# Kernel tuning notes

Hardware: AMD Instinct MI355X
Metric: run time of the kernel (lower is better)

## Reference

```python
import jax, jax.numpy as jnp
import numpy as np

N_NODES = 50000
N_EDGES = 800000
N_FEAT = 128
N_HID = 128
N_LAYER = 4
N_CLASS = 40


def setup_inputs() -> dict:
    key = jax.random.key(0)
    ks = jax.random.split(key, 8)
    x = jax.random.normal(ks[0], (N_NODES, N_FEAT), jnp.float32)
    edge_index = jax.random.randint(ks[1], (2, N_EDGES), 0, N_NODES, dtype=jnp.int64)
    s = 1.0 / np.float32(np.sqrt(N_HID))
    # n_feat == n_hid so all L conv weights stack into one [L, C, C] tensor
    convW = jax.random.normal(ks[2], (N_LAYER, N_HID, N_HID), jnp.float32) * s
    convb = jnp.zeros((N_LAYER, N_HID), jnp.float32)
    W_att = jax.random.normal(ks[3], (N_HID, N_HID), jnp.float32) * s
    a_att = jax.random.normal(ks[4], (N_HID,), jnp.float32) * s
    W_out = jax.random.normal(ks[5], (N_HID, N_CLASS), jnp.float32) * s
    b_out = jnp.zeros((N_CLASS,), jnp.float32)
    return dict(x=x, edge_index=edge_index, convW=convW, convb=convb,
                W_att=W_att, a_att=a_att, W_out=W_out, b_out=b_out)


def reference(x, edge_index, convW, convb, W_att, a_att, W_out, b_out):
    src, dst = edge_index[0], edge_index[1]
    N = x.shape[0]
    # GCN symmetric normalization with self-loops: deg = 1 + in-degree
    deg = jax.ops.segment_sum(jnp.ones_like(dst, dtype=jnp.float32), dst,
                              num_segments=N) + 1.0
    dinv = jax.lax.rsqrt(deg)
    enorm = (dinv[src] * dinv[dst])[:, None]   # per-edge norm
    snorm = (dinv * dinv)[:, None]             # self-loop norm

    hs = []
    h = x
    for l in range(N_LAYER):
        hW = h @ convW[l]                                          # [N, C]
        agg = jax.ops.segment_sum(hW[src] * enorm, dst, num_segments=N)
        agg = agg + hW * snorm                                     # self-loop
        h = jax.nn.relu(agg + convb[l])
        # dropout is identity at inference (training=False)
        hs.append(h)

    H = jnp.stack(hs, axis=1)                                      # [N, L, C]
    # additive attention over layers: alpha_l = softmax_l(a . tanh(W h_l))
    scores = jnp.tanh(H @ W_att) @ a_att                           # [N, L]
    alpha = jax.nn.softmax(scores, axis=1)
    fused = jnp.einsum('nl,nlc->nc', alpha, H)                     # [N, C]
    return fused @ W_out + b_out                                   # [N, n_class]
```

## Files before the change

kernel.cpp:

```cpp
#include <hip/hip_runtime.h>

#define NNODES 50000
#define NEDGES 800000
#define NCLASS 40
#define CNTB  3125
#define PREPB 320
#define WOUTB 24
#define GEMMB 782
#define XBLK  3125
#define WELL  64

typedef _Float16 half8  __attribute__((ext_vector_type(8)));
typedef float    floatx4 __attribute__((ext_vector_type(4)));

#define CSTR 136
#define SMEM_BYTES (64 * CSTR * 2 + 256)

__device__ __forceinline__ float fast_tanh(float x) {
    return 1.0f - 2.0f / (__expf(2.0f * x) + 1.0f);
}

__global__ __launch_bounds__(256) void k_pre(const int* __restrict__ src, const int* __restrict__ dst,
                                             int* __restrict__ cnt, int* __restrict__ esrc,
                                             const float* __restrict__ convW, const float* __restrict__ W_att,
                                             _Float16* __restrict__ WT,
                                             const float* __restrict__ Wout, _Float16* __restrict__ WoutT) {
    int bid = blockIdx.x, tid = threadIdx.x;
    if (bid < CNTB) {
        int e = bid * 256 + tid;
        int d = dst[e];
        int slot = atomicAdd(&cnt[d], 1);
        esrc[d * WELL + slot] = src[e];
    } else if (bid < CNTB + PREPB) {
        int idx = (bid - CNTB) * 256 + tid;
        int mat = idx >> 14, rem = idx & 16383;
        int j = rem & 7, lane = (rem >> 3) & 63, tile = rem >> 9;
        int l15 = lane & 15, quad = lane >> 4;
        int ct = tile & 7, kk = tile >> 3;
        int n = ct * 16 + l15, k = kk * 32 + quad * 8 + j;
        const float* s = (mat < 4) ? (convW + mat * 16384) : W_att;
        WT[idx] = (_Float16)s[k * 128 + n];
    } else {
        int idx = (bid - CNTB - PREPB) * 256 + tid;
        int j = idx & 7, lane = (idx >> 3) & 63, tile = idx >> 9;
        int l15 = lane & 15, quad = lane >> 4;
        int ct = tile % 3, kk = tile / 3;
        int n = ct * 16 + l15, k = kk * 32 + quad * 8 + j;
        WoutT[idx] = (n < NCLASS) ? (_Float16)Wout[k * NCLASS + n] : (_Float16)0.f;
    }
}

__global__ __launch_bounds__(256) void k_gemm0(const float* __restrict__ Av, const _Float16* __restrict__ WTf,
                                               const int* __restrict__ cnt, _Float16* __restrict__ C) {
    __shared__ __align__(16) char smem[SMEM_BYTES];
    _Float16 (*Csh)[CSTR] = (_Float16 (*)[CSTR])smem;
    float* sdinv = (float*)(smem + 64 * CSTR * 2);
    int m0 = blockIdx.x * 64;
    int tid = threadIdx.x;
    int wave = tid >> 6, lane = tid & 63;
    int quad = lane >> 4, l15 = lane & 15;
    int ko = quad * 8;

    if (tid < 64) {
        int r = m0 + tid; if (r > NNODES - 1) r = NNODES - 1;
        sdinv[tid] = rsqrtf((float)cnt[r] + 1.0f);
    }

    floatx4 acc[4][2];
#pragma unroll
    for (int rt = 0; rt < 4; ++rt)
#pragma unroll
        for (int ct = 0; ct < 2; ++ct) acc[rt][ct] = (floatx4){0.f, 0.f, 0.f, 0.f};

#pragma unroll
    for (int kk = 0; kk < 4; ++kk) {
        half8 a[4], b[2];
#pragma unroll
        for (int rt = 0; rt < 4; ++rt) {
            int row = m0 + rt * 16 + l15;
            if (row > NNODES - 1) row = NNODES - 1;
            const float* Ap = Av + (size_t)row * 128 + kk * 32 + ko;
            float4 f0 = *(const float4*)Ap;
            float4 f1 = *(const float4*)(Ap + 4);
            a[rt] = (half8){(_Float16)f0.x, (_Float16)f0.y, (_Float16)f0.z, (_Float16)f0.w,
                            (_Float16)f1.x, (_Float16)f1.y, (_Float16)f1.z, (_Float16)f1.w};
        }
#pragma unroll
        for (int ct = 0; ct < 2; ++ct)
            b[ct] = *(const half8*)&WTf[((kk * 8 + (wave * 2 + ct)) * 64 + lane) * 8];
#pragma unroll
        for (int rt = 0; rt < 4; ++rt)
#pragma unroll
            for (int ct = 0; ct < 2; ++ct)
                acc[rt][ct] = __builtin_amdgcn_mfma_f32_16x16x32_f16(a[rt], b[ct], acc[rt][ct], 0, 0, 0);
    }
    __syncthreads();

#pragma unroll
    for (int rt = 0; rt < 4; ++rt)
#pragma unroll
        for (int r = 0; r < 4; ++r) {
            float d = sdinv[rt * 16 + quad * 4 + r];
#pragma unroll
            for (int ct = 0; ct < 2; ++ct)
                Csh[rt * 16 + quad * 4 + r][wave * 32 + ct * 16 + l15] = (_Float16)(acc[rt][ct][r] * d);
        }
    __syncthreads();

    int row = tid >> 2, seg = tid & 3;
    int gm = m0 + row;
    if (gm < NNODES) {
#pragma unroll
        for (int j = 0; j < 4; ++j)
            *(half8*)(C + (size_t)gm * 128 + seg * 32 + j * 8) = *(const half8*)&Csh[row][seg * 32 + j * 8];
    }
}

template <bool HAS_GEMM>
__global__ __launch_bounds__(128) void k_layer(const _Float16* __restrict__ hin,
                                               const int* __restrict__ cnt, const int* __restrict__ esrc,
                                               const float* __restrict__ bias,
                                               _Float16* __restrict__ hh,
                                               const _Float16* __restrict__ WTatt, const float* __restrict__ a_att,
                                               float* __restrict__ scores, int layer,
                                               const _Float16* __restrict__ WTnext, _Float16* __restrict__ hout) {
    __shared__ __align__(16) _Float16 h[16][CSTR];
    __shared__ float bsh[128];
    __shared__ float sdv[16];
    __shared__ float pp[2][16];
    int tid = threadIdx.x;
    bsh[tid] = bias[tid];
    int wave = tid >> 6, lane = tid & 63;
    int n0 = blockIdx.x * 16;

    {
        int nl = tid >> 3;
        int cl = tid & 7;
        int c16 = cl * 16;
        int n = n0 + nl;
        int cv = cnt[n];
        int beg = n * WELL, end = beg + cv;
        float dn = rsqrtf((float)cv + 1.0f);
        const _Float16* sp = hin + (size_t)n * 128 + c16;
        half8 sv0 = *(const half8*)sp;
        half8 sv1 = *(const half8*)(sp + 8);

        float a[16];
#pragma unroll
        for (int u = 0; u < 16; ++u) a[u] = 0.f;

        int idxA[4]; float mskA[4];
#pragma unroll
        for (int i = 0; i < 4; ++i) {
            int ei = beg + i;
            int t = esrc[ei];
            bool ok = ei < end;
            idxA[i] = ok ? t : n;
            mskA[i] = ok ? 1.f : 0.f;
        }
        for (int e = beg; e < end; e += 4) {
            half8 v0[4], v1[4];
#pragma unroll
            for (int i = 0; i < 4; ++i) {
                const _Float16* p = hin + (size_t)idxA[i] * 128 + c16;
                v0[i] = *(const half8*)p;
                v1[i] = *(const half8*)(p + 8);
            }
            int idxB[4]; float mskB[4];
#pragma unroll
            for (int i = 0; i < 4; ++i) {
                int ei = e + 4 + i;
                int t = esrc[ei];
                bool ok = ei < end;
                idxB[i] = ok ? t : n;
                mskB[i] = ok ? 1.f : 0.f;
            }
#pragma unroll
            for (int i = 0; i < 4; ++i) {
                float m = mskA[i];
#pragma unroll
                for (int u = 0; u < 8; ++u) {
                    a[u]     += m * (float)v0[i][u];
                    a[8 + u] += m * (float)v1[i][u];
                }
            }
#pragma unroll
            for (int i = 0; i < 4; ++i) { idxA[i] = idxB[i]; mskA[i] = mskB[i]; }
        }
        __syncthreads();
        half8 o0, o1;
#pragma unroll
        for (int u = 0; u < 8; ++u) {
            float r0 = (a[u]     + (float)sv0[u]) * dn + bsh[c16 + u];
            float r1 = (a[8 + u] + (float)sv1[u]) * dn + bsh[c16 + 8 + u];
            o0[u] = (_Float16)fmaxf(r0, 0.f);
            o1[u] = (_Float16)fmaxf(r1, 0.f);
        }
        *(half8*)(hh + (size_t)n * 128 + c16)     = o0;
        *(half8*)(hh + (size_t)n * 128 + c16 + 8) = o1;
        *(half8*)&h[nl][c16]     = o0;
        *(half8*)&h[nl][c16 + 8] = o1;
        if (cl == 0) sdv[nl] = dn;
    }
    __syncthreads();

    int quad = lane >> 4, l15 = lane & 15;
    int ko = quad * 8;
    half8 af[4];
#pragma unroll
    for (int kk = 0; kk < 4; ++kk) af[kk] = *(const half8*)&h[l15][kk * 32 + ko];

    {
        float p[4] = {0.f, 0.f, 0.f, 0.f};
#pragma unroll
        for (int c2 = 0; c2 < 4; ++c2) {
            int ct = wave * 4 + c2;
            half8 b[4];
#pragma unroll
            for (int kk = 0; kk < 4; ++kk)
                b[kk] = *(const half8*)&WTatt[((kk * 8 + ct) * 64 + lane) * 8];
            floatx4 acc = (floatx4){0.f, 0.f, 0.f, 0.f};
#pragma unroll
            for (int kk = 0; kk < 4; ++kk)
                acc = __builtin_amdgcn_mfma_f32_16x16x32_f16(af[kk], b[kk], acc, 0, 0, 0);
            float av = a_att[ct * 16 + l15];
#pragma unroll
            for (int r = 0; r < 4; ++r) p[r] += av * fast_tanh(acc[r]);
        }
#pragma unroll
        for (int r = 0; r < 4; ++r) {
            float v = p[r];
            v += __shfl_xor(v, 1); v += __shfl_xor(v, 2);
            v += __shfl_xor(v, 4); v += __shfl_xor(v, 8);
            if (l15 == 0) pp[wave][quad * 4 + r] = v;
        }
    }
    __syncthreads();
    if (tid < 16) scores[(size_t)(n0 + tid) * 4 + layer] = pp[0][tid] + pp[1][tid];

    if (HAS_GEMM) {
        floatx4 acc[4];
#pragma unroll
        for (int c2 = 0; c2 < 4; ++c2) acc[c2] = (floatx4){0.f, 0.f, 0.f, 0.f};
#pragma unroll
        for (int c2 = 0; c2 < 4; ++c2) {
            int ct = wave * 4 + c2;
#pragma unroll
            for (int kk = 0; kk < 4; ++kk) {
                half8 b = *(const half8*)&WTnext[((kk * 8 + ct) * 64 + lane) * 8];
                acc[c2] = __builtin_amdgcn_mfma_f32_16x16x32_f16(af[kk], b, acc[c2], 0, 0, 0);
            }
        }
        __syncthreads();
#pragma unroll
        for (int c2 = 0; c2 < 4; ++c2) {
            int col = wave * 64 + c2 * 16 + l15;
#pragma unroll
            for (int r = 0; r < 4; ++r) {
                int row = quad * 4 + r;
                h[row][col] = (_Float16)(acc[c2][r] * sdv[row]);
            }
        }
        __syncthreads();
        int row = tid >> 3, seg = tid & 7;
        int gm = n0 + row;
        *(half8*)(hout + (size_t)gm * 128 + seg * 16)     = *(const half8*)&h[row][seg * 16];
        *(half8*)(hout + (size_t)gm * 128 + seg * 16 + 8) = *(const half8*)&h[row][seg * 16 + 8];
    }
}

__global__ __launch_bounds__(256) void k_fuse_out(const _Float16* __restrict__ hbase, const float* __restrict__ scores,
                                                  const _Float16* __restrict__ WoutT, const float* __restrict__ bout,
                                                  float* __restrict__ out) {
    __shared__ __align__(16) _Float16 Fs[64][136];
    __shared__ float salpha[256];
    const size_t LSTR = (size_t)NNODES * 128;
    int tid = threadIdx.x;
    int n0 = blockIdx.x * 64;

    if (tid < 64) {
        int node = n0 + tid; if (node > NNODES - 1) node = NNODES - 1;
        float4 s = *(const float4*)(scores + (size_t)node * 4);
        float mx = fmaxf(fmaxf(s.x, s.y), fmaxf(s.z, s.w));
        float e0 = __expf(s.x - mx), e1 = __expf(s.y - mx), e2 = __expf(s.z - mx), e3 = __expf(s.w - mx);
        float inv = 1.0f / (e0 + e1 + e2 + e3);
        salpha[tid * 4 + 0] = e0 * inv; salpha[tid * 4 + 1] = e1 * inv;
        salpha[tid * 4 + 2] = e2 * inv; salpha[tid * 4 + 3] = e3 * inv;
    }
    __syncthreads();

    {
        int no = tid >> 2, seg = tid & 3;
        int node = n0 + no; if (node > NNODES - 1) node = NNODES - 1;
        float al0 = salpha[no * 4 + 0], al1 = salpha[no * 4 + 1];
        float al2 = salpha[no * 4 + 2], al3 = salpha[no * 4 + 3];
        const _Float16* hp = hbase + (size_t)node * 128 + seg * 32;
#pragma unroll
        for (int j = 0; j < 4; ++j) {
            half8 h0 = *(const half8*)(hp + 0 * LSTR + j * 8);
            half8 h1 = *(const half8*)(hp + 1 * LSTR + j * 8);
            half8 h2 = *(const half8*)(hp + 2 * LSTR + j * 8);
            half8 h3 = *(const half8*)(hp + 3 * LSTR + j * 8);
            half8 f;
#pragma unroll
            for (int u = 0; u < 8; ++u)
                f[u] = (_Float16)(al0 * (float)h0[u] + al1 * (float)h1[u] +
                                  al2 * (float)h2[u] + al3 * (float)h3[u]);
            *(half8*)&Fs[no][seg * 32 + j * 8] = f;
        }
    }
    __syncthreads();

    int wave = tid >> 6, lane = tid & 63;
    int quad = lane >> 4, l15 = lane & 15;
    int ko = quad * 8;
    half8 ff[4];
    int frow = wave * 16 + l15;
#pragma unroll
    for (int kk = 0; kk < 4; ++kk) ff[kk] = *(const half8*)&Fs[frow][kk * 32 + ko];
#pragma unroll
    for (int ct = 0; ct < 3; ++ct) {
        half8 bw[4];
#pragma unroll
        for (int kk = 0; kk < 4; ++kk)
            bw[kk] = *(const half8*)(WoutT + ((kk * 3 + ct) * 64 + lane) * 8);
        floatx4 acc = (floatx4){0.f, 0.f, 0.f, 0.f};
#pragma unroll
        for (int kk = 0; kk < 4; ++kk)
            acc = __builtin_amdgcn_mfma_f32_16x16x32_f16(ff[kk], bw[kk], acc, 0, 0, 0);
        int col = ct * 16 + l15;
        if (col < NCLASS) {
            float bv = bout[col];
#pragma unroll
            for (int r = 0; r < 4; ++r) {
                int node = n0 + wave * 16 + quad * 4 + r;
                if (node < NNODES) out[(size_t)node * NCLASS + col] = acc[r] + bv;
            }
        }
    }
}

extern "C" void kernel_launch(void* const* d_in, const int* in_sizes, int n_in,
                              void* d_out, int out_size, void* d_ws, size_t ws_size,
                              hipStream_t stream) {
    const float* x     = (const float*)d_in[0];
    const int*   ei    = (const int*)d_in[1];
    const float* convW = (const float*)d_in[2];
    const float* convb = (const float*)d_in[3];
    const float* W_att = (const float*)d_in[4];
    const float* a_att = (const float*)d_in[5];
    const float* W_out = (const float*)d_in[6];
    const float* b_out = (const float*)d_in[7];
    float* out = (float*)d_out;

    char* ws = (char*)d_ws;
    size_t off = 0;
    auto take = [&](size_t nbytes) { char* p = ws + off; off += (nbytes + 255) & ~(size_t)255; return p; };
    int*       cnt     = (int*)take(NNODES * 4);
    int*       esrc    = (int*)take((size_t)NNODES * WELL * 4 + 1024);
    _Float16*  WoutT   = (_Float16*)take((size_t)48 * 128 * 2);
    float*     scores  = (float*)take(NNODES * 4 * 4);
    _Float16*  WT      = (_Float16*)take((size_t)5 * 128 * 128 * 2);
    _Float16*  hWsA    = (_Float16*)take((size_t)NNODES * 128 * 2);
    _Float16*  hh[4];
    for (int l = 0; l < 4; ++l) hh[l] = (_Float16*)take((size_t)NNODES * 128 * 2);
    _Float16*  hWsB    = (_Float16*)take((size_t)NNODES * 128 * 2);

    const int* src = ei;
    const int* dst = ei + NEDGES;

    hipMemsetAsync(cnt, 0, NNODES * 4, stream);
    k_pre<<<CNTB + PREPB + WOUTB, 256, 0, stream>>>(src, dst, cnt, esrc, convW, W_att, WT, W_out, WoutT);
    k_gemm0<<<GEMMB, 256, 0, stream>>>(x, WT, cnt, hWsA);

    k_layer<true><<<XBLK, 128, 0, stream>>>(hWsA, cnt, esrc, convb + 0 * 128, hh[0],
                                            WT + 4 * 16384, a_att, scores, 0, WT + 1 * 16384, hWsB);
    k_layer<true><<<XBLK, 128, 0, stream>>>(hWsB, cnt, esrc, convb + 1 * 128, hh[1],
                                            WT + 4 * 16384, a_att, scores, 1, WT + 2 * 16384, hWsA);
    k_layer<true><<<XBLK, 128, 0, stream>>>(hWsA, cnt, esrc, convb + 2 * 128, hh[2],
                                            WT + 4 * 16384, a_att, scores, 2, WT + 3 * 16384, hWsB);
    k_layer<false><<<XBLK, 128, 0, stream>>>(hWsB, cnt, esrc, convb + 3 * 128, hh[3],
                                             WT + 4 * 16384, a_att, scores, 3, (const _Float16*)nullptr,
                                             (_Float16*)nullptr);
    k_fuse_out<<<GEMMB, 256, 0, stream>>>(hh[0], scores, WoutT, b_out, out);
}
```

Measured before the change: 326.7 us.

## Replace global-atomic edge bucketing with two-level bucketed partition and local build

```diff
diff --git a/kernel.cpp b/kernel.cpp
--- a/kernel.cpp
+++ b/kernel.cpp
@@ -3,13 +3,18 @@
 #define NNODES 50000
 #define NEDGES 800000
 #define NCLASS 40
-#define CNTB  3125
-#define PREPB 320
-#define WOUTB 24
 #define GEMMB 782
 #define XBLK  3125
 #define WELL  64
 
+#define EBLK  782
+#define PREPB 80
+#define WOUTB 6
+#define BSHIFT 10
+#define NB    49
+#define NCNT  (NB * EBLK)
+#define SCANB 38
+
 typedef _Float16 half8  __attribute__((ext_vector_type(8)));
 typedef float    floatx4 __attribute__((ext_vector_type(4)));
 
@@ -20,19 +25,21 @@
     return 1.0f - 2.0f / (__expf(2.0f * x) + 1.0f);
 }
 
-__global__ __launch_bounds__(256) void k_pre(const int* __restrict__ src, const int* __restrict__ dst,
-                                             int* __restrict__ cnt, int* __restrict__ esrc,
-                                             const float* __restrict__ convW, const float* __restrict__ W_att,
-                                             _Float16* __restrict__ WT,
-                                             const float* __restrict__ Wout, _Float16* __restrict__ WoutT) {
+__global__ __launch_bounds__(1024) void k_hist(const int* __restrict__ dst, int* __restrict__ counts,
+                                               const float* __restrict__ convW, const float* __restrict__ W_att,
+                                               _Float16* __restrict__ WT,
+                                               const float* __restrict__ Wout, _Float16* __restrict__ WoutT) {
     int bid = blockIdx.x, tid = threadIdx.x;
-    if (bid < CNTB) {
-        int e = bid * 256 + tid;
-        int d = dst[e];
-        int slot = atomicAdd(&cnt[d], 1);
-        esrc[d * WELL + slot] = src[e];
-    } else if (bid < CNTB + PREPB) {
-        int idx = (bid - CNTB) * 256 + tid;
+    if (bid < EBLK) {
+        __shared__ int hist[NB];
+        if (tid < NB) hist[tid] = 0;
+        __syncthreads();
+        int e = bid * 1024 + tid;
+        if (e < NEDGES) atomicAdd(&hist[dst[e] >> BSHIFT], 1);
+        __syncthreads();
+        if (tid < NB) counts[tid * EBLK + bid] = hist[tid];
+    } else if (bid < EBLK + PREPB) {
+        int idx = (bid - EBLK) * 1024 + tid;
         int mat = idx >> 14, rem = idx & 16383;
         int j = rem & 7, lane = (rem >> 3) & 63, tile = rem >> 9;
         int l15 = lane & 15, quad = lane >> 4;
@@ -41,13 +48,91 @@
         const float* s = (mat < 4) ? (convW + mat * 16384) : W_att;
         WT[idx] = (_Float16)s[k * 128 + n];
     } else {
-        int idx = (bid - CNTB - PREPB) * 256 + tid;
+        int idx = (bid - EBLK - PREPB) * 1024 + tid;
         int j = idx & 7, lane = (idx >> 3) & 63, tile = idx >> 9;
         int l15 = lane & 15, quad = lane >> 4;
         int ct = tile % 3, kk = tile / 3;
         int n = ct * 16 + l15, k = kk * 32 + quad * 8 + j;
         WoutT[idx] = (n < NCLASS) ? (_Float16)Wout[k * NCLASS + n] : (_Float16)0.f;
     }
+}
+
+__global__ __launch_bounds__(1024) void k_bsum(const int* __restrict__ counts, int* __restrict__ bsum) {
+    int t = threadIdx.x, b = blockIdx.x;
+    int i = b * 1024 + t;
+    int v = (i < NCNT) ? counts[i] : 0;
+    v += __shfl_xor(v, 1);  v += __shfl_xor(v, 2);  v += __shfl_xor(v, 4);
+    v += __shfl_xor(v, 8);  v += __shfl_xor(v, 16); v += __shfl_xor(v, 32);
+    __shared__ int ws[16];
+    if ((t & 63) == 0) ws[t >> 6] = v;
+    __syncthreads();
+    if (t == 0) {
+        int s = 0;
+#pragma unroll
+        for (int w = 0; w < 16; ++w) s += ws[w];
+        bsum[b] = s;
+    }
+}
+
+__global__ __launch_bounds__(1024) void k_scan(int* __restrict__ counts, const int* __restrict__ bsum) {
+    __shared__ int part[1024];
+    __shared__ int ws[16];
+    int t = threadIdx.x, b = blockIdx.x;
+    int i = b * 1024 + t;
+    int c = (i < NCNT) ? counts[i] : 0;
+    int pv = (t < b) ? bsum[t] : 0;
+    pv += __shfl_xor(pv, 1);  pv += __shfl_xor(pv, 2);  pv += __shfl_xor(pv, 4);
+    pv += __shfl_xor(pv, 8);  pv += __shfl_xor(pv, 16); pv += __shfl_xor(pv, 32);
+    if ((t & 63) == 0) ws[t >> 6] = pv;
+    part[t] = c;
+    __syncthreads();
+    int boff = 0;
+#pragma unroll
+    for (int w = 0; w < 16; ++w) boff += ws[w];
+#pragma unroll
+    for (int d = 1; d < 1024; d <<= 1) {
+        int v = (t >= d) ? part[t - d] : 0;
+        __syncthreads();
+        part[t] += v;
+        __syncthreads();
+    }
+    if (i < NCNT) counts[i] = boff + part[t] - c;
+}
+
+__global__ __launch_bounds__(1024) void k_part(const int* __restrict__ src, const int* __restrict__ dst,
+                                               const int* __restrict__ counts, int2* __restrict__ ebuf) {
+    __shared__ int hist2[NB];
+    int bid = blockIdx.x, tid = threadIdx.x;
+    if (tid < NB) hist2[tid] = 0;
+    __syncthreads();
+    int e = bid * 1024 + tid;
+    if (e < NEDGES) {
+        int d = dst[e];
+        int s = src[e];
+        int b = d >> BSHIFT;
+        int slot = atomicAdd(&hist2[b], 1);
+        int pos = counts[b * EBLK + bid] + slot;
+        ebuf[pos] = make_int2(s, d);
+    }
+}
+
+__global__ __launch_bounds__(1024) void k_build(const int* __restrict__ counts, const int2* __restrict__ ebuf,
+                                                int* __restrict__ esrc, int* __restrict__ cnt) {
+    __shared__ int lcnt[1024];
+    int b = blockIdx.x, t = threadIdx.x;
+    lcnt[t] = 0;
+    __syncthreads();
+    int n0 = b << BSHIFT;
+    int lo = counts[b * EBLK];
+    int hi = (b < NB - 1) ? counts[(b + 1) * EBLK] : NEDGES;
+    for (int i = lo + t; i < hi; i += 1024) {
+        int2 p = ebuf[i];
+        int slot = atomicAdd(&lcnt[p.y - n0], 1);
+        esrc[p.y * WELL + slot] = p.x;
+    }
+    __syncthreads();
+    int n = n0 + t;
+    if (n < NNODES) cnt[n] = lcnt[t];
 }
 
 __global__ __launch_bounds__(256) void k_gemm0(const float* __restrict__ Av, const _Float16* __restrict__ WTf,
@@ -357,6 +442,9 @@
     size_t off = 0;
     auto take = [&](size_t nbytes) { char* p = ws + off; off += (nbytes + 255) & ~(size_t)255; return p; };
     int*       cnt     = (int*)take(NNODES * 4);
+    int*       counts  = (int*)take((size_t)NCNT * 4);
+    int*       bsum    = (int*)take(SCANB * 4);
+    int2*      ebuf    = (int2*)take((size_t)NEDGES * 8);
     int*       esrc    = (int*)take((size_t)NNODES * WELL * 4 + 1024);
     _Float16*  WoutT   = (_Float16*)take((size_t)48 * 128 * 2);
     float*     scores  = (float*)take(NNODES * 4 * 4);
@@ -369,8 +457,11 @@
     const int* src = ei;
     const int* dst = ei + NEDGES;
 
-    hipMemsetAsync(cnt, 0, NNODES * 4, stream);
-    k_pre<<<CNTB + PREPB + WOUTB, 256, 0, stream>>>(src, dst, cnt, esrc, convW, W_att, WT, W_out, WoutT);
+    k_hist<<<EBLK + PREPB + WOUTB, 1024, 0, stream>>>(dst, counts, convW, W_att, WT, W_out, WoutT);
+    k_bsum<<<SCANB, 1024, 0, stream>>>(counts, bsum);
+    k_scan<<<SCANB, 1024, 0, stream>>>(counts, bsum);
+    k_part<<<EBLK, 1024, 0, stream>>>(src, dst, counts, ebuf);
+    k_build<<<NB, 1024, 0, stream>>>(counts, ebuf, esrc, cnt);
     k_gemm0<<<GEMMB, 256, 0, stream>>>(x, WT, cnt, hWsA);
 
     k_layer<true><<<XBLK, 128, 0, stream>>>(hWsA, cnt, esrc, convb + 0 * 128, hh[0],
```

New measurement: 303.4 us. 7.1% less time.

## Build destination-bucketed edge lists via two-pass partition instead of global atomics

Applied to the files above, without the earlier changes.

```diff
diff --git a/kernel.cpp b/kernel.cpp
--- a/kernel.cpp
+++ b/kernel.cpp
@@ -3,13 +3,17 @@
 #define NNODES 50000
 #define NEDGES 800000
 #define NCLASS 40
-#define CNTB  3125
-#define PREPB 320
-#define WOUTB 24
 #define GEMMB 782
 #define XBLK  3125
 #define WELL  64
 
+#define EBLK  782
+#define PREPB 80
+#define WOUTB 6
+#define BSHIFT 10
+#define NB    49
+#define BUCKCAP 20480
+
 typedef _Float16 half8  __attribute__((ext_vector_type(8)));
 typedef float    floatx4 __attribute__((ext_vector_type(4)));
 
@@ -20,19 +24,35 @@
     return 1.0f - 2.0f / (__expf(2.0f * x) + 1.0f);
 }
 
-__global__ __launch_bounds__(256) void k_pre(const int* __restrict__ src, const int* __restrict__ dst,
-                                             int* __restrict__ cnt, int* __restrict__ esrc,
-                                             const float* __restrict__ convW, const float* __restrict__ W_att,
-                                             _Float16* __restrict__ WT,
-                                             const float* __restrict__ Wout, _Float16* __restrict__ WoutT) {
+__global__ __launch_bounds__(1024) void k_part(const int* __restrict__ src, const int* __restrict__ dst,
+                                               int* __restrict__ gbase, int2* __restrict__ ebuf,
+                                               const float* __restrict__ convW, const float* __restrict__ W_att,
+                                               _Float16* __restrict__ WT,
+                                               const float* __restrict__ Wout, _Float16* __restrict__ WoutT) {
     int bid = blockIdx.x, tid = threadIdx.x;
-    if (bid < CNTB) {
-        int e = bid * 256 + tid;
-        int d = dst[e];
-        int slot = atomicAdd(&cnt[d], 1);
-        esrc[d * WELL + slot] = src[e];
-    } else if (bid < CNTB + PREPB) {
-        int idx = (bid - CNTB) * 256 + tid;
+    if (bid < EBLK) {
+        __shared__ int hist[NB];
+        __shared__ int base[NB];
+        if (tid < NB) hist[tid] = 0;
+        __syncthreads();
+        int e = bid * 1024 + tid;
+        bool ok = e < NEDGES;
+        int s = 0, d = 0, b = 0, slot = 0;
+        if (ok) {
+            d = dst[e];
+            s = src[e];
+            b = d >> BSHIFT;
+            slot = atomicAdd(&hist[b], 1);
+        }
+        __syncthreads();
+        if (tid < NB) base[tid] = atomicAdd(&gbase[tid * 32], hist[tid]);
+        __syncthreads();
+        if (ok) {
+            int pos = base[b] + slot;
+            if (pos < BUCKCAP) ebuf[(size_t)b * BUCKCAP + pos] = make_int2(s, d);
+        }
+    } else if (bid < EBLK + PREPB) {
+        int idx = (bid - EBLK) * 1024 + tid;
         int mat = idx >> 14, rem = idx & 16383;
         int j = rem & 7, lane = (rem >> 3) & 63, tile = rem >> 9;
         int l15 = lane & 15, quad = lane >> 4;
@@ -41,13 +61,33 @@
         const float* s = (mat < 4) ? (convW + mat * 16384) : W_att;
         WT[idx] = (_Float16)s[k * 128 + n];
     } else {
-        int idx = (bid - CNTB - PREPB) * 256 + tid;
+        int idx = (bid - EBLK - PREPB) * 1024 + tid;
         int j = idx & 7, lane = (idx >> 3) & 63, tile = idx >> 9;
         int l15 = lane & 15, quad = lane >> 4;
         int ct = tile % 3, kk = tile / 3;
         int n = ct * 16 + l15, k = kk * 32 + quad * 8 + j;
         WoutT[idx] = (n < NCLASS) ? (_Float16)Wout[k * NCLASS + n] : (_Float16)0.f;
     }
+}
+
+__global__ __launch_bounds__(1024) void k_build(const int* __restrict__ gbase, const int2* __restrict__ ebuf,
+                                                int* __restrict__ esrc, int* __restrict__ cnt) {
+    __shared__ int lcnt[1024];
+    int b = blockIdx.x, t = threadIdx.x;
+    lcnt[t] = 0;
+    __syncthreads();
+    int n0 = b << BSHIFT;
+    int total = gbase[b * 32];
+    if (total > BUCKCAP) total = BUCKCAP;
+    const int2* ep = ebuf + (size_t)b * BUCKCAP;
+    for (int i = t; i < total; i += 1024) {
+        int2 p = ep[i];
+        int slot = atomicAdd(&lcnt[p.y - n0], 1);
+        if (slot < WELL) esrc[p.y * WELL + slot] = p.x;
+    }
+    __syncthreads();
+    int n = n0 + t;
+    if (n < NNODES) cnt[n] = (lcnt[t] < WELL) ? lcnt[t] : WELL;
 }
 
 __global__ __launch_bounds__(256) void k_gemm0(const float* __restrict__ Av, const _Float16* __restrict__ WTf,
@@ -357,6 +397,8 @@
     size_t off = 0;
     auto take = [&](size_t nbytes) { char* p = ws + off; off += (nbytes + 255) & ~(size_t)255; return p; };
     int*       cnt     = (int*)take(NNODES * 4);
+    int*       gbase   = (int*)take((size_t)NB * 32 * 4);
+    int2*      ebuf    = (int2*)take((size_t)NB * BUCKCAP * 8);
     int*       esrc    = (int*)take((size_t)NNODES * WELL * 4 + 1024);
     _Float16*  WoutT   = (_Float16*)take((size_t)48 * 128 * 2);
     float*     scores  = (float*)take(NNODES * 4 * 4);
@@ -369,8 +411,9 @@
     const int* src = ei;
     const int* dst = ei + NEDGES;
 
-    hipMemsetAsync(cnt, 0, NNODES * 4, stream);
-    k_pre<<<CNTB + PREPB + WOUTB, 256, 0, stream>>>(src, dst, cnt, esrc, convW, W_att, WT, W_out, WoutT);
+    hipMemsetAsync(gbase, 0, (size_t)NB * 32 * 4, stream);
+    k_part<<<EBLK + PREPB + WOUTB, 1024, 0, stream>>>(src, dst, gbase, ebuf, convW, W_att, WT, W_out, WoutT);
+    k_build<<<NB, 1024, 0, stream>>>(gbase, ebuf, esrc, cnt);
     k_gemm0<<<GEMMB, 256, 0, stream>>>(x, WT, cnt, hWsA);
 
     k_layer<true><<<XBLK, 128, 0, stream>>>(hWsA, cnt, esrc, convb + 0 * 128, hh[0],
```

New measurement: 303.0 us. 7.3% less time.
